# Kernel tuning notes

Measured on AMD Instinct MI355X. Metric: run time of the kernel, lower is better.

## Reference

```python
import jax, jax.numpy as jnp
import numpy as np

B, FEAT, FIELD, K = 16384, 2048, 32, 64

def setup_inputs() -> dict:
    key = jax.random.key(0)
    k1, k2, k3, k4 = jax.random.split(key, 4)
    x = jax.random.normal(k1, (B, FEAT), dtype=jnp.float32)
    # nn.Linear(feature_size, 1): weight [1, FEAT] (use vector), bias [1] (scalar)
    w = jax.random.normal(k2, (FEAT,), dtype=jnp.float32) / np.sqrt(FEAT)
    b = jax.random.normal(k3, (), dtype=jnp.float32)
    # v ~ N(0, 0.01) as in torch.normal(0, 0.01, ...)
    v = 0.01 * jax.random.normal(k4, (FEAT, FIELD, K), dtype=jnp.float32)
    return {"x": x, "w": w, "b": b, "v": v}

def reference(x, w, b, v):
    # linear part: Linear(feature_size, 1).squeeze() -> [B]
    linear_part = x @ w + b  # [B]
    # field_x = tensordot(x, v, dims=1) -> [B, FIELD, K]
    field_x = jnp.einsum('bf,fsk->bsk', x, v)
    # sum_{i<j} sum_k f_i * f_j  ==  0.5 * (||sum_i f_i||^2 - sum_i ||f_i||^2)
    s = field_x.sum(axis=1)                      # [B, K]
    sq = (field_x * field_x).sum(axis=(1, 2))    # [B]
    interaction = 0.5 * ((s * s).sum(axis=-1) - sq)  # [B]
    return jax.nn.sigmoid(linear_part + interaction)
```

## Files before the change

kernel.cpp:

```cpp
#include <hip/hip_runtime.h>
#include <cstdint>
#include <cstddef>

#define B_ROWS 16384
#define FEAT   2048
#define FIELD  32
#define KDIM   64
#define NCOLS  2048
#define NAUG   2176

using half8   = __attribute__((ext_vector_type(8))) _Float16;
using half4   = __attribute__((ext_vector_type(4))) _Float16;
using floatx4 = __attribute__((ext_vector_type(4))) float;

__device__ __forceinline__ void load_lds16(const void* g, void* l) {
  __builtin_amdgcn_global_load_lds((const __attribute__((address_space(1))) void*)g,
                                   (__attribute__((address_space(3))) void*)l, 16, 0, 0);
}

__global__ __launch_bounds__(256) void k_prep_x(const float* __restrict__ x,
                                                _Float16* __restrict__ xh) {
  const int bb = blockIdx.x;
  const int t = threadIdx.x;
  size_t i = ((size_t)bb * 256 + t) * 16;
  float4 v0 = *(const float4*)(x + i);
  float4 v1 = *(const float4*)(x + i + 4);
  float4 v2 = *(const float4*)(x + i + 8);
  float4 v3 = *(const float4*)(x + i + 12);
  half8 h0 = { (_Float16)v0.x, (_Float16)v0.y, (_Float16)v0.z, (_Float16)v0.w,
               (_Float16)v1.x, (_Float16)v1.y, (_Float16)v1.z, (_Float16)v1.w };
  half8 h1 = { (_Float16)v2.x, (_Float16)v2.y, (_Float16)v2.z, (_Float16)v2.w,
               (_Float16)v3.x, (_Float16)v3.y, (_Float16)v3.z, (_Float16)v3.w };
  *(half8*)(xh + i) = h0;
  *(half8*)(xh + i + 8) = h1;
}

__global__ __launch_bounds__(256) void k_prep_v(const float* __restrict__ v,
                                                const float* __restrict__ w,
                                                _Float16* __restrict__ vt,
                                                float* __restrict__ arg) {
  const int bb = blockIdx.x;
  const int t = threadIdx.x;
  if (bb < 1024) {
    __shared__ _Float16 tile[64 * 68];
    const int f0 = (bb >> 5) * 64;
    const int n0 = (bb & 31) * 64;
#pragma unroll
    for (int j = 0; j < 4; ++j) {
      int c = j * 256 + t;
      int row = c >> 4;
      int col = (c & 15) * 4;
      float4 val = *(const float4*)(v + (size_t)(f0 + row) * NCOLS + n0 + col);
      tile[row * 68 + col + 0] = (_Float16)val.x;
      tile[row * 68 + col + 1] = (_Float16)val.y;
      tile[row * 68 + col + 2] = (_Float16)val.z;
      tile[row * 68 + col + 3] = (_Float16)val.w;
    }
    __syncthreads();
#pragma unroll
    for (int j = 0; j < 4; ++j) {
      int c = j * 256 + t;
      int nl = c >> 4;
      int fl = (c & 15) * 4;
      half4 h = { tile[(fl + 0) * 68 + nl], tile[(fl + 1) * 68 + nl],
                  tile[(fl + 2) * 68 + nl], tile[(fl + 3) * 68 + nl] };
      *(half4*)(vt + (size_t)(n0 + nl) * FEAT + f0 + fl) = h;
    }
  } else if (bb < 1536) {
    const int k = t & 63;
    const int f = (bb - 1024) * 4 + (t >> 6);
    float s = 0.f;
#pragma unroll
    for (int si = 0; si < FIELD; ++si) s += v[(size_t)f * NCOLS + si * KDIM + k];
    vt[(size_t)(NCOLS + k) * FEAT + f] = (_Float16)s;
  } else if (bb < 2048) {
    int idx = (bb - 1536) * 256 + t;
    int r = NCOLS + KDIM + (idx >> 11);
    int f = idx & 2047;
    vt[(size_t)r * FEAT + f] = (r == NCOLS + KDIM) ? (_Float16)w[f] : (_Float16)0.f;
  } else {
    arg[(bb - 2048) * 256 + t] = 0.f;
  }
}

__global__ __launch_bounds__(512, 2) void k_gemm(const _Float16* __restrict__ xh,
                                                 const _Float16* __restrict__ vt,
                                                 float* __restrict__ arg) {
  __shared__ __align__(16) _Float16 lds[65536];
  const int tid  = threadIdx.x;
  const int lane = tid & 63;
  const int wave = tid >> 6;
  const int wm   = wave >> 2;
  const int wn   = wave & 3;
  const int lr   = lane & 15;
  const int q    = lane >> 4;

  const int bid = blockIdx.x;
  const int wg  = (bid & 7) * 64 + (bid >> 3);
  const int ng  = wg >> 7;
  const int rem = wg & 127;
  const int mi  = rem >> 1;
  const int nr  = rem & 1;
  const int m0  = mi * 256;
  const int n0  = (ng * 2 + nr) * 256;

  int offA[4], offB[4];
#pragma unroll
  for (int f = 0; f < 4; ++f) {
    int L = f * 16 + lr;
    int u = wm * 4 + q;
    offA[f] = L * 64 + ((u ^ (L & 7)) * 8);
  }
#pragma unroll
  for (int g = 0; g < 4; ++g) {
    int L = (wn & 1) * 64 + g * 16 + lr;
    int u = (wn >> 1) * 4 + q;
    offB[g] = L * 64 + ((u ^ (L & 7)) * 8);
  }

  const int L0   = tid >> 3;
  const int u0   = (tid & 7) ^ (L0 & 7);
  const int row0 = (u0 >> 2) * 128 + L0;
  const int kc0  = u0 & 3;
  const _Float16* pA0 = xh + (size_t)(m0 + row0) * FEAT + kc0 * 8;
  const _Float16* pA1 = pA0 + (size_t)64 * FEAT;
  const _Float16* pB0 = vt + (size_t)(n0 + row0) * FEAT + kc0 * 8;
  const _Float16* pB1 = pB0 + (size_t)64 * FEAT;

  auto stageA = [&](int koff, int seg) {
    load_lds16(pA0 + koff, lds + seg + tid * 8);
    load_lds16(pA1 + koff, lds + seg + 4096 + tid * 8);
  };
  auto stageB = [&](int koff, int seg) {
    load_lds16(pB0 + koff, lds + seg + tid * 8);
    load_lds16(pB1 + koff, lds + seg + 4096 + tid * 8);
  };

  floatx4 acc[8][4] = {};
  half8 af[4], bf[4];

  stageA(0, 0);       stageB(0, 32768);
  stageA(32, 8192);   stageB(32, 40960);
  stageA(64, 16384);  stageB(64, 49152);
  asm volatile("s_waitcnt vmcnt(4)" ::: "memory");
  __builtin_amdgcn_s_barrier();

#define PHASE_TAIL()                                        \
    __builtin_amdgcn_s_barrier();                           \
    asm volatile("s_waitcnt lgkmcnt(0)" ::: "memory");      \
    __builtin_amdgcn_sched_barrier(0);                      \
    __builtin_amdgcn_s_setprio(1)

#define PHASE_END()                                         \
    __builtin_amdgcn_s_setprio(0);                          \
    __builtin_amdgcn_s_barrier()

#pragma unroll 2
  for (int t = 0; t < 32; ++t) {
    const int sA0  = ((t & 1) << 1) * 8192;
    const int sB0  = 32768 + sA0;
    const int sPA1 = ((((t + 1) & 1) << 1) | 1) * 8192;

#pragma unroll
    for (int g = 0; g < 4; ++g) bf[g] = *(const half8*)(lds + sB0 + offB[g]);
#pragma unroll
    for (int f = 0; f < 4; ++f) af[f] = *(const half8*)(lds + sA0 + offA[f]);
    if (t < 31) stageA((t + 1) * 64 + 32, sPA1);
    PHASE_TAIL();
#pragma unroll
    for (int f = 0; f < 4; ++f)
#pragma unroll
      for (int g = 0; g < 4; ++g)
        acc[f][g] = __builtin_amdgcn_mfma_f32_16x16x32_f16(af[f], bf[g],
                                                           acc[f][g], 0, 0, 0);
    PHASE_END();

#pragma unroll
    for (int f = 0; f < 4; ++f) af[f] = *(const half8*)(lds + sA0 + 4096 + offA[f]);
    if (t < 31) stageB((t + 1) * 64 + 32, 32768 + sPA1);
    PHASE_TAIL();
#pragma unroll
    for (int f = 0; f < 4; ++f)
#pragma unroll
      for (int g = 0; g < 4; ++g)
        acc[4 + f][g] = __builtin_amdgcn_mfma_f32_16x16x32_f16(af[f], bf[g],
                                                               acc[4 + f][g], 0, 0, 0);
    PHASE_END();

#pragma unroll
    for (int g = 0; g < 4; ++g) bf[g] = *(const half8*)(lds + sB0 + 8192 + offB[g]);
#pragma unroll
    for (int f = 0; f < 4; ++f) af[f] = *(const half8*)(lds + sA0 + 8192 + offA[f]);
    if (t < 30) stageA((t + 2) * 64, sA0);
    PHASE_TAIL();
#pragma unroll
    for (int f = 0; f < 4; ++f)
#pragma unroll
      for (int g = 0; g < 4; ++g)
        acc[f][g] = __builtin_amdgcn_mfma_f32_16x16x32_f16(af[f], bf[g],
                                                           acc[f][g], 0, 0, 0);
    PHASE_END();

#pragma unroll
    for (int f = 0; f < 4; ++f) af[f] = *(const half8*)(lds + sA0 + 12288 + offA[f]);
    if (t < 30) stageB((t + 2) * 64, sB0);
    __builtin_amdgcn_s_barrier();
    asm volatile("s_waitcnt lgkmcnt(0)" ::: "memory");
    __builtin_amdgcn_sched_barrier(0);
    __builtin_amdgcn_s_setprio(1);
#pragma unroll
    for (int f = 0; f < 4; ++f)
#pragma unroll
      for (int g = 0; g < 4; ++g)
        acc[4 + f][g] = __builtin_amdgcn_mfma_f32_16x16x32_f16(af[f], bf[g],
                                                               acc[4 + f][g], 0, 0, 0);
    __builtin_amdgcn_s_setprio(0);
    if (t < 30) { asm volatile("s_waitcnt vmcnt(4)" ::: "memory"); }
    else        { asm volatile("s_waitcnt vmcnt(0)" ::: "memory"); }
    __builtin_amdgcn_sched_barrier(0);
    __builtin_amdgcn_s_barrier();
  }
#undef PHASE_TAIL
#undef PHASE_END

  const int cq = lane >> 4;
  const int mrow = m0 + wm * 128;
#pragma unroll
  for (int f = 0; f < 8; ++f) {
#pragma unroll
    for (int r = 0; r < 4; ++r) {
      float contrib = 0.f;
#pragma unroll
      for (int g = 0; g < 4; ++g) {
        float vv = acc[f][g][r];
        contrib -= 0.5f * vv * vv;
      }
      contrib += __shfl_xor(contrib, 1);
      contrib += __shfl_xor(contrib, 2);
      contrib += __shfl_xor(contrib, 4);
      contrib += __shfl_xor(contrib, 8);
      if (lr == 0) atomicAdd(&arg[mrow + f * 16 + cq * 4 + r], contrib);
    }
  }
}

__global__ __launch_bounds__(256) void k_fin_aug(const _Float16* __restrict__ xh,
                                                 const _Float16* __restrict__ vt,
                                                 const float* __restrict__ arg,
                                                 const float* __restrict__ b,
                                                 float* __restrict__ out) {
  __shared__ __align__(16) _Float16 lds_a[64 * 64];
  __shared__ __align__(16) _Float16 lds_b[128 * 64];
  __shared__ float augp[64];
  const int t = threadIdx.x;
  const int m0 = blockIdx.x * 64;
  const int lane = t & 63;
  const int wave = t >> 6;
  const int wm = (wave & 1) * 32;
  const int wn = (wave >> 1) * 64;
  const int lr = lane & 15;
  const int lk = (lane >> 4) * 8;

  if (t < 64) augp[t] = 0.f;

  floatx4 acc[2][4] = {};

  for (int k0 = 0; k0 < FEAT; k0 += 64) {
#pragma unroll
    for (int i = 0; i < 2; ++i) {
      int c = i * 256 + t;
      int row = c >> 3;
      int g = (c & 7) ^ (row & 7);
      load_lds16(xh + (size_t)(m0 + row) * FEAT + k0 + g * 8, lds_a + c * 8);
    }
#pragma unroll
    for (int i = 0; i < 4; ++i) {
      int c = i * 256 + t;
      int row = c >> 3;
      int g = (c & 7) ^ (row & 7);
      load_lds16(vt + (size_t)(NCOLS + row) * FEAT + k0 + g * 8, lds_b + c * 8);
    }
    __syncthreads();
#pragma unroll
    for (int ks = 0; ks < 64; ks += 32) {
      const int kc = (ks + lk) >> 3;
      half8 af[2], bf[4];
#pragma unroll
      for (int f = 0; f < 2; ++f) {
        int ma = wm + f * 16 + lr;
        af[f] = *(const half8*)(lds_a + ma * 64 + (kc ^ (ma & 7)) * 8);
      }
#pragma unroll
      for (int f = 0; f < 4; ++f) {
        int nb = wn + f * 16 + lr;
        bf[f] = *(const half8*)(lds_b + nb * 64 + (kc ^ (nb & 7)) * 8);
      }
#pragma unroll
      for (int fm = 0; fm < 2; ++fm)
#pragma unroll
        for (int fn = 0; fn < 4; ++fn)
          acc[fm][fn] = __builtin_amdgcn_mfma_f32_16x16x32_f16(af[fm], bf[fn],
                                                               acc[fm][fn], 0, 0, 0);
    }
    __syncthreads();
  }

  const int cq = lane >> 4;
#pragma unroll
  for (int fm = 0; fm < 2; ++fm) {
#pragma unroll
    for (int r = 0; r < 4; ++r) {
      float contrib = 0.f;
#pragma unroll
      for (int fn = 0; fn < 4; ++fn) {
        int col = wn + fn * 16 + lr;
        float vv = acc[fm][fn][r];
        if (col < KDIM)            contrib += 0.5f * vv * vv;
        else if (col == KDIM)      contrib += vv;
      }
      contrib += __shfl_xor(contrib, 1);
      contrib += __shfl_xor(contrib, 2);
      contrib += __shfl_xor(contrib, 4);
      contrib += __shfl_xor(contrib, 8);
      if (lr == 0) atomicAdd(&augp[wm + fm * 16 + cq * 4 + r], contrib);
    }
  }
  __syncthreads();
  if (t < 64) {
    float z = arg[m0 + t] + augp[t] + b[0];
    out[m0 + t] = 1.f / (1.f + __expf(-z));
  }
}

extern "C" void kernel_launch(void* const* d_in, const int* in_sizes, int n_in,
                              void* d_out, int out_size, void* d_ws, size_t ws_size,
                              hipStream_t stream) {
  const float* x = (const float*)d_in[0];
  const float* w = (const float*)d_in[1];
  const float* b = (const float*)d_in[2];
  const float* v = (const float*)d_in[3];
  float* out = (float*)d_out;

  char* ws = (char*)d_ws;
  _Float16* xh  = (_Float16*)ws;
  _Float16* vt  = (_Float16*)(ws + 67108864);
  float*    arg = (float*)(ws + 67108864 + 8912896);

  k_prep_x<<<8192, 256, 0, stream>>>(x, xh);
  k_prep_v<<<2112, 256, 0, stream>>>(v, w, vt, arg);
  k_gemm<<<512, 512, 0, stream>>>(xh, vt, arg);
  k_fin_aug<<<256, 256, 0, stream>>>(xh, vt, arg, b, out);
}
```

Before: 374.7 us.

## Fuse x fp16 conversion with augmented-column GEMM into one prep kernel

Merges the x-to-fp16 conversion kernel with the auxiliary GEMM over the sum-of-fields and linear columns. The converted tile is written to global memory and also placed straight into LDS for the MFMA work. The final kernel shrinks to an elementwise sigmoid. This avoids re-reading xh from global in the old aux kernel, at the cost of a smaller 32-row tile, synchronous loads with no overlap, and atomics into arg before the main GEMM.

```diff
diff --git a/kernel.cpp b/kernel.cpp
--- a/kernel.cpp
+++ b/kernel.cpp
@@ -16,23 +16,6 @@
 __device__ __forceinline__ void load_lds16(const void* g, void* l) {
   __builtin_amdgcn_global_load_lds((const __attribute__((address_space(1))) void*)g,
                                    (__attribute__((address_space(3))) void*)l, 16, 0, 0);
-}
-
-__global__ __launch_bounds__(256) void k_prep_x(const float* __restrict__ x,
-                                                _Float16* __restrict__ xh) {
-  const int bb = blockIdx.x;
-  const int t = threadIdx.x;
-  size_t i = ((size_t)bb * 256 + t) * 16;
-  float4 v0 = *(const float4*)(x + i);
-  float4 v1 = *(const float4*)(x + i + 4);
-  float4 v2 = *(const float4*)(x + i + 8);
-  float4 v3 = *(const float4*)(x + i + 12);
-  half8 h0 = { (_Float16)v0.x, (_Float16)v0.y, (_Float16)v0.z, (_Float16)v0.w,
-               (_Float16)v1.x, (_Float16)v1.y, (_Float16)v1.z, (_Float16)v1.w };
-  half8 h1 = { (_Float16)v2.x, (_Float16)v2.y, (_Float16)v2.z, (_Float16)v2.w,
-               (_Float16)v3.x, (_Float16)v3.y, (_Float16)v3.z, (_Float16)v3.w };
-  *(half8*)(xh + i) = h0;
-  *(half8*)(xh + i + 8) = h1;
 }
 
 __global__ __launch_bounds__(256) void k_prep_v(const float* __restrict__ v,
@@ -80,6 +63,82 @@
     vt[(size_t)r * FEAT + f] = (r == NCOLS + KDIM) ? (_Float16)w[f] : (_Float16)0.f;
   } else {
     arg[(bb - 2048) * 256 + t] = 0.f;
+  }
+}
+
+__global__ __launch_bounds__(256) void k_prep_xa(const float* __restrict__ x,
+                                                 const _Float16* __restrict__ vt,
+                                                 _Float16* __restrict__ xh,
+                                                 float* __restrict__ arg) {
+  __shared__ __align__(16) _Float16 lds_a[32 * 64];
+  __shared__ __align__(16) _Float16 lds_b[128 * 64];
+  const int t = threadIdx.x;
+  const int m0 = blockIdx.x * 32;
+  const int lane = t & 63;
+  const int wave = t >> 6;
+  const int wm = (wave & 1) * 16;
+  const int wn = (wave >> 1) * 64;
+  const int lr = lane & 15;
+  const int lk = (lane >> 4) * 8;
+
+  const int arow = t >> 3;
+  const int akc  = t & 7;
+  const float*    xsrc = x  + (size_t)(m0 + arow) * FEAT + akc * 8;
+  _Float16*       xdst = xh + (size_t)(m0 + arow) * FEAT + akc * 8;
+  _Float16*       adst = lds_a + arow * 64 + (akc ^ (arow & 7)) * 8;
+
+  floatx4 acc[4] = {};
+
+  for (int k0 = 0; k0 < FEAT; k0 += 64) {
+    float4 va = *(const float4*)(xsrc + k0);
+    float4 vb = *(const float4*)(xsrc + k0 + 4);
+    half8 h = { (_Float16)va.x, (_Float16)va.y, (_Float16)va.z, (_Float16)va.w,
+                (_Float16)vb.x, (_Float16)vb.y, (_Float16)vb.z, (_Float16)vb.w };
+    *(half8*)(xdst + k0) = h;
+    *(half8*)adst = h;
+#pragma unroll
+    for (int i = 0; i < 4; ++i) {
+      int c = i * 256 + t;
+      int row = c >> 3;
+      int g = (c & 7) ^ (row & 7);
+      load_lds16(vt + (size_t)(NCOLS + row) * FEAT + k0 + g * 8, lds_b + c * 8);
+    }
+    __syncthreads();
+#pragma unroll
+    for (int ks = 0; ks < 64; ks += 32) {
+      const int kc = (ks + lk) >> 3;
+      const int ma = wm + lr;
+      half8 af = *(const half8*)(lds_a + ma * 64 + (kc ^ (ma & 7)) * 8);
+      half8 bf[4];
+#pragma unroll
+      for (int f = 0; f < 4; ++f) {
+        int nb = wn + f * 16 + lr;
+        bf[f] = *(const half8*)(lds_b + nb * 64 + (kc ^ (nb & 7)) * 8);
+      }
+#pragma unroll
+      for (int fn = 0; fn < 4; ++fn)
+        acc[fn] = __builtin_amdgcn_mfma_f32_16x16x32_f16(af, bf[fn],
+                                                         acc[fn], 0, 0, 0);
+    }
+    __syncthreads();
+  }
+
+  const int cq = lane >> 4;
+#pragma unroll
+  for (int r = 0; r < 4; ++r) {
+    float contrib = 0.f;
+#pragma unroll
+    for (int fn = 0; fn < 4; ++fn) {
+      int col = wn + fn * 16 + lr;
+      float vv = acc[fn][r];
+      if (col < KDIM)            contrib += 0.5f * vv * vv;
+      else if (col == KDIM)      contrib += vv;
+    }
+    contrib += __shfl_xor(contrib, 1);
+    contrib += __shfl_xor(contrib, 2);
+    contrib += __shfl_xor(contrib, 4);
+    contrib += __shfl_xor(contrib, 8);
+    if (lr == 0) atomicAdd(&arg[m0 + wm + cq * 4 + r], contrib);
   }
 }
 
@@ -244,92 +303,12 @@
   }
 }
 
-__global__ __launch_bounds__(256) void k_fin_aug(const _Float16* __restrict__ xh,
-                                                 const _Float16* __restrict__ vt,
-                                                 const float* __restrict__ arg,
-                                                 const float* __restrict__ b,
-                                                 float* __restrict__ out) {
-  __shared__ __align__(16) _Float16 lds_a[64 * 64];
-  __shared__ __align__(16) _Float16 lds_b[128 * 64];
-  __shared__ float augp[64];
-  const int t = threadIdx.x;
-  const int m0 = blockIdx.x * 64;
-  const int lane = t & 63;
-  const int wave = t >> 6;
-  const int wm = (wave & 1) * 32;
-  const int wn = (wave >> 1) * 64;
-  const int lr = lane & 15;
-  const int lk = (lane >> 4) * 8;
-
-  if (t < 64) augp[t] = 0.f;
-
-  floatx4 acc[2][4] = {};
-
-  for (int k0 = 0; k0 < FEAT; k0 += 64) {
-#pragma unroll
-    for (int i = 0; i < 2; ++i) {
-      int c = i * 256 + t;
-      int row = c >> 3;
-      int g = (c & 7) ^ (row & 7);
-      load_lds16(xh + (size_t)(m0 + row) * FEAT + k0 + g * 8, lds_a + c * 8);
-    }
-#pragma unroll
-    for (int i = 0; i < 4; ++i) {
-      int c = i * 256 + t;
-      int row = c >> 3;
-      int g = (c & 7) ^ (row & 7);
-      load_lds16(vt + (size_t)(NCOLS + row) * FEAT + k0 + g * 8, lds_b + c * 8);
-    }
-    __syncthreads();
-#pragma unroll
-    for (int ks = 0; ks < 64; ks += 32) {
-      const int kc = (ks + lk) >> 3;
-      half8 af[2], bf[4];
-#pragma unroll
-      for (int f = 0; f < 2; ++f) {
-        int ma = wm + f * 16 + lr;
-        af[f] = *(const half8*)(lds_a + ma * 64 + (kc ^ (ma & 7)) * 8);
-      }
-#pragma unroll
-      for (int f = 0; f < 4; ++f) {
-        int nb = wn + f * 16 + lr;
-        bf[f] = *(const half8*)(lds_b + nb * 64 + (kc ^ (nb & 7)) * 8);
-      }
-#pragma unroll
-      for (int fm = 0; fm < 2; ++fm)
-#pragma unroll
-        for (int fn = 0; fn < 4; ++fn)
-          acc[fm][fn] = __builtin_amdgcn_mfma_f32_16x16x32_f16(af[fm], bf[fn],
-                                                               acc[fm][fn], 0, 0, 0);
-    }
-    __syncthreads();
-  }
-
-  const int cq = lane >> 4;
-#pragma unroll
-  for (int fm = 0; fm < 2; ++fm) {
-#pragma unroll
-    for (int r = 0; r < 4; ++r) {
-      float contrib = 0.f;
-#pragma unroll
-      for (int fn = 0; fn < 4; ++fn) {
-        int col = wn + fn * 16 + lr;
-        float vv = acc[fm][fn][r];
-        if (col < KDIM)            contrib += 0.5f * vv * vv;
-        else if (col == KDIM)      contrib += vv;
-      }
-      contrib += __shfl_xor(contrib, 1);
-      contrib += __shfl_xor(contrib, 2);
-      contrib += __shfl_xor(contrib, 4);
-      contrib += __shfl_xor(contrib, 8);
-      if (lr == 0) atomicAdd(&augp[wm + fm * 16 + cq * 4 + r], contrib);
-    }
-  }
-  __syncthreads();
-  if (t < 64) {
-    float z = arg[m0 + t] + augp[t] + b[0];
-    out[m0 + t] = 1.f / (1.f + __expf(-z));
-  }
+__global__ __launch_bounds__(256) void k_fin(const float* __restrict__ arg,
+                                             const float* __restrict__ b,
+                                             float* __restrict__ out) {
+  int i = blockIdx.x * 256 + threadIdx.x;
+  float z = arg[i] + b[0];
+  out[i] = 1.f / (1.f + __expf(-z));
 }
 
 extern "C" void kernel_launch(void* const* d_in, const int* in_sizes, int n_in,
@@ -346,8 +325,8 @@
   _Float16* vt  = (_Float16*)(ws + 67108864);
   float*    arg = (float*)(ws + 67108864 + 8912896);
 
-  k_prep_x<<<8192, 256, 0, stream>>>(x, xh);
   k_prep_v<<<2112, 256, 0, stream>>>(v, w, vt, arg);
+  k_prep_xa<<<512, 256, 0, stream>>>(x, vt, xh, arg);
   k_gemm<<<512, 512, 0, stream>>>(xh, vt, arg);
-  k_fin_aug<<<256, 256, 0, stream>>>(xh, vt, arg, b, out);
-}
+  k_fin<<<64, 256, 0, stream>>>(arg, b, out);
+}
```

Result: faster. 354.9 us (-5.3%).
